# Performance work log

Measured on AMD Instinct MI355X. Metric: run time of the kernel, lower is better.

Reference implementation:

```python
import jax, jax.numpy as jnp
import numpy as np

# Model constants (from init_kwargs / _select_heads)
H = 8          # heads for dim=1024
KR = 16        # read/write top-k
CHUNK = 128    # chunk size for chunked memory update
ETA = 0.1      # update rate
FORGET = 0.01  # decay_lambda -> forget_base per chunk
LWIN = 512     # local_window = K (use_bypass=True)


def _l2norm(t, eps=1e-6):
    return t / (jnp.linalg.norm(t, axis=-1, keepdims=True) + eps)


def setup_inputs() -> dict:
    key = jax.random.key(0)
    ks = jax.random.split(key, 5)
    B, T, D, K = 2, 2048, 1024, 512
    x = jax.random.normal(ks[0], (B, T, D), dtype=jnp.float32)
    W_qkv = jax.random.normal(ks[1], (3 * D, D), dtype=jnp.float32) / np.sqrt(D)
    b_qkv = jnp.zeros((3 * D,), dtype=jnp.float32)
    W_o = jax.random.normal(ks[2], (D, D), dtype=jnp.float32) / np.sqrt(D)
    b_o = jnp.zeros((D,), dtype=jnp.float32)
    S_init = jax.random.normal(ks[3], (K, D), dtype=jnp.float32) / np.sqrt(D)
    read_temperature = jnp.ones((1,), dtype=jnp.float32)
    return {"x": x, "W_qkv": W_qkv, "b_qkv": b_qkv, "W_o": W_o,
            "b_o": b_o, "S_init": S_init, "read_temperature": read_temperature}


def reference(x, W_qkv, b_qkv, W_o, b_o, S_init, read_temperature):
    B, T, D = x.shape
    K = S_init.shape[0]
    dh = D // H
    scale = 1.0 / np.sqrt(dh)
    temp = read_temperature[0]

    # fused qkv projection, split to heads [B,H,T,dh]
    qkv = x @ W_qkv.T + b_qkv
    q, k, v = jnp.split(qkv, 3, axis=-1)
    to_h = lambda t: t.reshape(B, T, H, dh).transpose(0, 2, 1, 3)
    qh, kh, vh = to_h(q), to_h(k), to_h(v)

    # initial slot state from S_init: [K, D] -> [H, K, dh] -> [B,H,K,dh]
    slot = S_init.reshape(K, H, dh).transpose(1, 0, 2)
    slot_k0 = jnp.broadcast_to(_l2norm(slot), (B, H, K, dh))
    slot_v0 = jnp.broadcast_to(slot, (B, H, K, dh))

    nc = T // CHUNK
    # [nc, B, H, C, dh]
    to_c = lambda t: t.reshape(B, H, nc, CHUNK, dh).transpose(2, 0, 1, 3, 4)
    qc, kc, vc = to_c(qh), to_c(kh), to_c(vh)

    bi_g = jnp.arange(B)[:, None, None, None]   # gather indices
    hi_g = jnp.arange(H)[None, :, None, None]
    bi_s = jnp.arange(B)[:, None, None]         # scatter indices
    hi_s = jnp.arange(H)[None, :, None]

    def chunk_step(carry, inp):
        slot_k, slot_v = carry
        qt, kt, vt = inp  # [B,H,C,dh]
        # ---- top-k sparse read from slot memory ----
        rscores = jnp.einsum('bhcd,bhkd->bhck', qt, slot_k) * scale / temp
        rv, ri = jax.lax.top_k(rscores, KR)
        rp = jax.nn.softmax(rv, axis=-1)                 # [B,H,C,KR]
        sel_v = slot_v[bi_g, hi_g, ri]                   # [B,H,C,KR,dh]
        read = jnp.einsum('bhck,bhckd->bhcd', rp, sel_v)
        # ---- top-k write with orthogonal update + decay ----
        k_hat = _l2norm(kt)
        wscores = jnp.einsum('bhcd,bhkd->bhck', k_hat, slot_k)
        wv, wi = jax.lax.top_k(wscores, KR)
        wp = jax.nn.softmax(wv, axis=-1)
        sel_k = slot_k[bi_g, hi_g, wi]                   # [B,H,C,KR,dh]
        proj = jnp.einsum('bhcd,bhckd->bhck', vt, sel_k)
        v_orth = vt[:, :, :, None, :] - proj[..., None] * sel_k
        dv = ETA * wp[..., None] * v_orth                # [B,H,C,KR,dh]
        dk = ETA * wp[..., None] * (k_hat[:, :, :, None, :] - sel_k)
        idx = wi.reshape(B, H, CHUNK * KR)
        slot_v = (1.0 - FORGET) * slot_v
        slot_v = slot_v.at[bi_s, hi_s, idx].add(dv.reshape(B, H, CHUNK * KR, dh))
        slot_k = _l2norm(slot_k.at[bi_s, hi_s, idx].add(dk.reshape(B, H, CHUNK * KR, dh)))
        return (slot_k, slot_v), read

    _, reads = jax.lax.scan(chunk_step, (slot_k0, slot_v0), (qc, kc, vc))
    reads = reads.transpose(1, 2, 0, 3, 4).reshape(B, H, T, dh)

    # ---- local bypass: block-causal sliding-window attention (window=LWIN) ----
    nb = T // LWIN
    qb = qh.reshape(B, H, nb, LWIN, dh)
    kb = kh.reshape(B, H, nb, LWIN, dh)
    vb = vh.reshape(B, H, nb, LWIN, dh)
    zpad = jnp.zeros_like(kb[:, :, :1])
    kcat = jnp.concatenate([jnp.concatenate([zpad, kb[:, :, :-1]], axis=2), kb], axis=3)
    vcat = jnp.concatenate([jnp.concatenate([zpad, vb[:, :, :-1]], axis=2), vb], axis=3)
    s = jnp.einsum('bhnqd,bhnkd->bhnqk', qb, kcat) * scale  # [B,H,nb,LWIN,2*LWIN]
    i = jnp.arange(LWIN)[:, None]
    j = jnp.arange(2 * LWIN)[None, :]
    base = (j <= LWIN + i) & (j > i)                        # causal + window
    blk = (jnp.arange(nb) > 0)[:, None, None] | (j >= LWIN)[None]
    mask = base[None] & blk                                 # [nb,LWIN,2*LWIN]
    s = jnp.where(mask[None, None], s, -1e30)
    a = jax.nn.softmax(s, axis=-1)
    local = jnp.einsum('bhnqk,bhnkd->bhnqd', a, vcat).reshape(B, H, T, dh)

    y = (reads + local).transpose(0, 2, 1, 3).reshape(B, T, D)
    return y @ W_o.T + b_o
```

## Files before the change

kernel.cpp:

```cpp
#include <hip/hip_runtime.h>

typedef unsigned short u16;
typedef unsigned int u32;
typedef unsigned long long u64;
typedef __attribute__((ext_vector_type(8))) short bf16x8;
typedef __attribute__((ext_vector_type(4))) float f32x4;

#define B2 2
#define T2 2048
#define D2 1024
#define H2 8
#define DH 128
#define KSL 512
#define CH 128
#define NCH 16
#define NBH 16
#define MAGIC 0x13579BDFu

__device__ __forceinline__ float bf2f(u32 h) { union { u32 u; float f; } x; x.u = h << 16; return x.f; }
__device__ __forceinline__ u16 f2bf(float f) {
  union { float f; u32 u; } x; x.f = f;
  return (u16)((x.u + 0x7FFFu + ((x.u >> 16) & 1u)) >> 16);
}
__device__ __forceinline__ u32 pack2(float a, float b) { return (u32)f2bf(a) | ((u32)f2bf(b) << 16); }

__device__ __forceinline__ u32 cload32(const void* p) {
  return __hip_atomic_load((u32*)p, __ATOMIC_RELAXED, __HIP_MEMORY_SCOPE_AGENT);
}
__device__ __forceinline__ void cstore32(void* p, u32 v) {
  __hip_atomic_store((u32*)p, v, __ATOMIC_RELAXED, __HIP_MEMORY_SCOPE_AGENT);
}
__device__ __forceinline__ u64 cload64(const void* p) {
  return __hip_atomic_load((u64*)p, __ATOMIC_RELAXED, __HIP_MEMORY_SCOPE_AGENT);
}
__device__ __forceinline__ void cstore64(void* p, u64 v) {
  __hip_atomic_store((u64*)p, v, __ATOMIC_RELAXED, __HIP_MEMORY_SCOPE_AGENT);
}
__device__ __forceinline__ float2 cloadf2(const float* p) {
  union { u64 q; float2 f; } x; x.q = cload64(p); return x.f;
}
__device__ __forceinline__ void cstoref2(float* p, float2 v) {
  union { float2 f; u64 q; } x; x.f = v; cstore64(p, x.q);
}

__global__ __launch_bounds__(256) void qkv_gemm(
    const float* __restrict__ x, const float* __restrict__ w,
    const float* __restrict__ bias, u16* __restrict__ qhb,
    u16* __restrict__ khb, u16* __restrict__ vhb) {
  __shared__ u16 As[128 * 72];
  __shared__ u16 Bs[128 * 72];
  const int tid = threadIdx.x;
  const int lane = tid & 63, wv = tid >> 6;
  const int quad = lane >> 4, l15 = lane & 15;
  const int m0 = blockIdx.y * 128, n0 = blockIdx.x * 128;
  const int wr = wv >> 1, wc = wv & 1;
  f32x4 acc[4][4];
#pragma unroll
  for (int i = 0; i < 4; ++i)
#pragma unroll
    for (int j = 0; j < 4; ++j) acc[i][j] = f32x4{0.f, 0.f, 0.f, 0.f};
  const int f4c = tid & 15, r0 = tid >> 4;
  for (int kt = 0; kt < 16; ++kt) {
#pragma unroll
    for (int i = 0; i < 8; ++i) {
      int row = r0 + i * 16;
      float4 a = *(const float4*)(x + (size_t)(m0 + row) * 1024 + kt * 64 + f4c * 4);
      float4 b = *(const float4*)(w + (size_t)(n0 + row) * 1024 + kt * 64 + f4c * 4);
      *(uint2*)(&As[row * 72 + f4c * 4]) = make_uint2(pack2(a.x, a.y), pack2(a.z, a.w));
      *(uint2*)(&Bs[row * 72 + f4c * 4]) = make_uint2(pack2(b.x, b.y), pack2(b.z, b.w));
    }
    __syncthreads();
#pragma unroll
    for (int ks = 0; ks < 2; ++ks) {
      bf16x8 af[4], bff[4];
#pragma unroll
      for (int rt = 0; rt < 4; ++rt)
        af[rt] = *(const bf16x8*)(&As[(wr * 64 + rt * 16 + l15) * 72 + ks * 32 + quad * 8]);
#pragma unroll
      for (int ct = 0; ct < 4; ++ct)
        bff[ct] = *(const bf16x8*)(&Bs[(wc * 64 + ct * 16 + l15) * 72 + ks * 32 + quad * 8]);
#pragma unroll
      for (int rt = 0; rt < 4; ++rt)
#pragma unroll
        for (int ct = 0; ct < 4; ++ct)
          acc[rt][ct] = __builtin_amdgcn_mfma_f32_16x16x32_bf16(af[rt], bff[ct], acc[rt][ct], 0, 0, 0);
    }
    __syncthreads();
  }
#pragma unroll
  for (int ct = 0; ct < 4; ++ct) {
    int n = n0 + wc * 64 + ct * 16 + l15;
    float bv = bias[n];
    int sec = n >> 10, rr2 = n & 1023, hh = rr2 >> 7, dd = rr2 & 127;
    u16* dst = (sec == 0) ? qhb : (sec == 1) ? khb : vhb;
#pragma unroll
    for (int rt = 0; rt < 4; ++rt)
#pragma unroll
      for (int rg = 0; rg < 4; ++rg) {
        int m = m0 + wr * 64 + rt * 16 + quad * 4 + rg;
        int bb = m >> 11, tt = m & 2047;
        dst[((size_t)(bb * 8 + hh) * T2 + tt) * DH + dd] = f2bf(acc[rt][ct][rg] + bv);
      }
  }
}

__global__ __launch_bounds__(256) void attn_kernel(
    const u16* __restrict__ qhb, const u16* __restrict__ khb,
    const u16* __restrict__ vhb, float* __restrict__ yin) {
  __shared__ u16 Pls[128 * 72];
  __shared__ u16 VT[128 * 72];
  const int tid = threadIdx.x;
  const int lane = tid & 63, wv = tid >> 6;
  const int quad = lane >> 4, l15 = lane & 15;
  const int bh = blockIdx.y, qt = blockIdx.x;
  const int t0 = qt * 128;
  const int b = bh >> 3, h = bh & 7;
  f32x4 Oa[2][8];
  float mrow[2][4], lrow[2][4];
#pragma unroll
  for (int rt = 0; rt < 2; ++rt) {
#pragma unroll
    for (int dt = 0; dt < 8; ++dt) Oa[rt][dt] = f32x4{0.f, 0.f, 0.f, 0.f};
#pragma unroll
    for (int rg = 0; rg < 4; ++rg) { mrow[rt][rg] = -1e30f; lrow[rt][rg] = 0.f; }
  }
  const u16* qbase = qhb + ((size_t)bh * T2 + t0) * DH;
  int j0 = t0 / 64 - 8; if (j0 < 0) j0 = 0;
  int j1 = t0 / 64 + 1;
  for (int jt = j0; jt <= j1; ++jt) {
    int kv0 = jt * 64;
    __syncthreads();
    {
      int r = tid & 63, dq = tid >> 6;
      const u16* vrow = vhb + ((size_t)bh * T2 + kv0 + r) * DH + dq * 32;
#pragma unroll
      for (int u = 0; u < 4; ++u) {
        uint4 pv = *(const uint4*)(vrow + u * 8);
        int d0 = dq * 32 + u * 8;
        VT[(d0 + 0) * 72 + r] = (u16)(pv.x); VT[(d0 + 1) * 72 + r] = (u16)(pv.x >> 16);
        VT[(d0 + 2) * 72 + r] = (u16)(pv.y); VT[(d0 + 3) * 72 + r] = (u16)(pv.y >> 16);
        VT[(d0 + 4) * 72 + r] = (u16)(pv.z); VT[(d0 + 5) * 72 + r] = (u16)(pv.z >> 16);
        VT[(d0 + 6) * 72 + r] = (u16)(pv.w); VT[(d0 + 7) * 72 + r] = (u16)(pv.w >> 16);
      }
    }
    f32x4 Sa[2][4];
#pragma unroll
    for (int rt = 0; rt < 2; ++rt)
#pragma unroll
      for (int ct = 0; ct < 4; ++ct) Sa[rt][ct] = f32x4{0.f, 0.f, 0.f, 0.f};
#pragma unroll
    for (int ks = 0; ks < 4; ++ks) {
      bf16x8 a0 = *(const bf16x8*)(qbase + (size_t)(wv * 32 + l15) * DH + ks * 32 + quad * 8);
      bf16x8 a1 = *(const bf16x8*)(qbase + (size_t)(wv * 32 + 16 + l15) * DH + ks * 32 + quad * 8);
#pragma unroll
      for (int ct = 0; ct < 4; ++ct) {
        bf16x8 bb = *(const bf16x8*)(khb + ((size_t)bh * T2 + kv0 + ct * 16 + l15) * DH + ks * 32 + quad * 8);
        Sa[0][ct] = __builtin_amdgcn_mfma_f32_16x16x32_bf16(a0, bb, Sa[0][ct], 0, 0, 0);
        Sa[1][ct] = __builtin_amdgcn_mfma_f32_16x16x32_bf16(a1, bb, Sa[1][ct], 0, 0, 0);
      }
    }
#pragma unroll
    for (int rt = 0; rt < 2; ++rt)
#pragma unroll
      for (int rg = 0; rg < 4; ++rg) {
        int row = wv * 32 + rt * 16 + quad * 4 + rg;
        int qp = t0 + row;
        float vals[4];
        float mx = -1e30f;
#pragma unroll
        for (int ct = 0; ct < 4; ++ct) {
          int kp = kv0 + ct * 16 + l15;
          float s = Sa[rt][ct][rg] * 0.08838834764831845f;
          bool ok = (kp <= qp) && (kp + 512 > qp);
          s = ok ? s : -1e30f;
          vals[ct] = s;
          mx = fmaxf(mx, s);
        }
#pragma unroll
        for (int sh = 1; sh < 16; sh <<= 1) mx = fmaxf(mx, __shfl_xor(mx, sh));
        float mold = mrow[rt][rg];
        float mnew = fmaxf(mold, mx);
        float alpha = __expf(mold - mnew);
        float rsum = 0.f;
        float pv_[4];
#pragma unroll
        for (int ct = 0; ct < 4; ++ct) {
          float p = (vals[ct] < -1e29f) ? 0.f : __expf(vals[ct] - mnew);
          pv_[ct] = p; rsum += p;
        }
#pragma unroll
        for (int sh = 1; sh < 16; sh <<= 1) rsum += __shfl_xor(rsum, sh);
        lrow[rt][rg] = lrow[rt][rg] * alpha + rsum;
        mrow[rt][rg] = mnew;
#pragma unroll
        for (int dt = 0; dt < 8; ++dt) Oa[rt][dt][rg] *= alpha;
#pragma unroll
        for (int ct = 0; ct < 4; ++ct) Pls[row * 72 + ct * 16 + l15] = f2bf(pv_[ct]);
      }
    __syncthreads();
#pragma unroll
    for (int ks = 0; ks < 2; ++ks) {
      bf16x8 a0 = *(const bf16x8*)(&Pls[(wv * 32 + l15) * 72 + ks * 32 + quad * 8]);
      bf16x8 a1 = *(const bf16x8*)(&Pls[(wv * 32 + 16 + l15) * 72 + ks * 32 + quad * 8]);
#pragma unroll
      for (int dt = 0; dt < 8; ++dt) {
        bf16x8 bb = *(const bf16x8*)(&VT[(dt * 16 + l15) * 72 + ks * 32 + quad * 8]);
        Oa[0][dt] = __builtin_amdgcn_mfma_f32_16x16x32_bf16(a0, bb, Oa[0][dt], 0, 0, 0);
        Oa[1][dt] = __builtin_amdgcn_mfma_f32_16x16x32_bf16(a1, bb, Oa[1][dt], 0, 0, 0);
      }
    }
  }
#pragma unroll
  for (int rt = 0; rt < 2; ++rt)
#pragma unroll
    for (int rg = 0; rg < 4; ++rg) {
      int row = wv * 32 + rt * 16 + quad * 4 + rg;
      float invl = 1.0f / lrow[rt][rg];
#pragma unroll
      for (int dt = 0; dt < 8; ++dt)
        yin[((size_t)b * T2 + t0 + row) * D2 + h * DH + dt * 16 + l15] = Oa[rt][dt][rg] * invl;
    }
}

struct ScanArgs {
  const u16* qhb; const u16* khb; const u16* vhb;
  float* yin; float* sk; float* sv; u16* skb; u16* khatb;
  u32* cnt; uint4* entries;
  u32* barcnt; u32* bargen; u32* ready;
  const float* sinit; const float* temp;
};

__device__ __forceinline__ void bh_barrier(u32* cnt, u32* gen, bool do_inv) {
  asm volatile("" ::: "memory");
  __syncthreads();
  if (threadIdx.x == 0) {
    u32 g = cload32(gen);
    u32 a = __hip_atomic_fetch_add(cnt, 1u, __ATOMIC_RELAXED, __HIP_MEMORY_SCOPE_AGENT);
    if ((a & 15u) == 15u) {
      cstore32(gen, g + 1u);
    } else {
      while (cload32(gen) == g) __builtin_amdgcn_s_sleep(2);
    }
    if (do_inv)
      __builtin_amdgcn_fence(__ATOMIC_ACQUIRE, "agent");
  }
  __syncthreads();
  asm volatile("" ::: "memory");
}

__device__ __forceinline__ void topk16(const float* rowp, int lane, volatile u64* candw,
                                       float& p_out, u32& idx_out) {
  u32 mono[8];
#pragma unroll
  for (int j = 0; j < 8; ++j) {
    float f = rowp[j * 64 + lane];
    u32 u = __float_as_uint(f);
    mono[j] = ((int)u < 0) ? ~u : (u | 0x80000000u);
  }
  u32 mx = mono[0];
#pragma unroll
  for (int j = 1; j < 8; ++j) mx = max(mx, mono[j]);
  u32 s = mx;
#pragma unroll
  for (int k = 2; k <= 64; k <<= 1) {
#pragma unroll
    for (int j = k >> 1; j > 0; j >>= 1) {
      u32 o = (u32)__shfl_xor((int)s, j);
      bool keep_min = (((lane & k) == 0) == ((lane & j) == 0));
      u32 mn = min(s, o), mxx = max(s, o);
      s = keep_min ? mn : mxx;
    }
  }
  u32 thr = (u32)__shfl((int)s, 48);
  u32 base = 0;
#pragma unroll
  for (int j = 0; j < 8; ++j) {
    bool pred = (mono[j] >= thr);
    u64 mask = __ballot(pred);
    u32 pos = base + (u32)__popcll(mask & ((1ull << lane) - 1ull));
    if (pred && pos < 64u)
      candw[pos] = (((u64)mono[j]) << 32) | (u64)(0xFFFFFFFFu - (u32)(j * 64 + lane));
    base += (u32)__popcll(mask);
  }
  __threadfence_block();
  u32 cntc = base < 64u ? base : 64u;
  u64 key = ((u32)lane < cntc) ? candw[lane] : 0ull;
#pragma unroll
  for (int k = 2; k <= 64; k <<= 1) {
#pragma unroll
    for (int j = k >> 1; j > 0; j >>= 1) {
      u64 o = __shfl_xor(key, j);
      bool keep_min = (((lane & k) == 0) == ((lane & j) == 0));
      u64 mn = key < o ? key : o;
      u64 mxx = key < o ? o : key;
      key = keep_min ? mn : mxx;
    }
  }
  u32 um = (u32)(key >> 32);
  float val = __uint_as_float((um & 0x80000000u) ? (um & 0x7FFFFFFFu) : ~um);
  idx_out = 0xFFFFFFFFu - (u32)(key & 0xFFFFFFFFull);
  float mtop = __shfl(val, 63);
  float e = __expf(val - mtop);
  float ssum = e;
#pragma unroll
  for (int sh = 1; sh < 16; sh <<= 1) ssum += __shfl_xor(ssum, sh);
  p_out = e / ssum;
}

__global__ __launch_bounds__(512, 2) void scan_kernel(ScanArgs A) {
  const int tid = threadIdx.x;
  const int lane = tid & 63, wv = tid >> 6;
  const int quad = lane >> 4, l15 = lane & 15;
  const int xcd = blockIdx.x & 7;
  const int wi = blockIdx.x >> 3;
  const int bh = xcd * 2 + (wi >> 4);
  const int blk = wi & 15;
  const int b = bh >> 3, h = bh & 7;
  __shared__ float scores_r[8 * 520];
  __shared__ float scores_w[8 * 520];
  __shared__ u64 cand[8][64];

  const float invtemp = 1.0f / A.temp[0];
  const float sc_r = 0.08838834764831845f * invtemp;

#pragma unroll 1
  for (int i = 0; i < 4; ++i) {
    int s = blk * 32 + wv * 4 + i;
    float2 v2 = *(const float2*)(A.sinit + (size_t)s * 1024 + h * 128 + lane * 2);
    float ssq = v2.x * v2.x + v2.y * v2.y;
#pragma unroll
    for (int sh = 1; sh < 64; sh <<= 1) ssq += __shfl_xor(ssq, sh);
    float inv = 1.0f / (sqrtf(ssq) + 1e-6f);
    size_t off = ((size_t)bh * KSL + s) * DH + lane * 2;
    cstoref2(A.sk + off, make_float2(v2.x * inv, v2.y * inv));
    cstoref2(A.sv + off, v2);
    cstore32(A.skb + off, pack2(v2.x * inv, v2.y * inv));
    if (lane == 0) cstore32(&A.cnt[bh * KSL + s], 0u);
  }
#pragma unroll 1
  for (int ci = 0; ci < NCH; ++ci) {
    int trow = ci * CH + blk * 8 + wv;
    u32 kraw = *(const u32*)(A.khb + ((size_t)bh * T2 + trow) * DH + lane * 2);
    float k0 = bf2f(kraw & 0xFFFFu), k1 = bf2f(kraw >> 16);
    float ssq = k0 * k0 + k1 * k1;
#pragma unroll
    for (int sh = 1; sh < 64; sh <<= 1) ssq += __shfl_xor(ssq, sh);
    float inv = 1.0f / (sqrtf(ssq) + 1e-6f);
    cstore32(A.khatb + ((size_t)bh * T2 + trow) * DH + lane * 2, pack2(k0 * inv, k1 * inv));
  }
  if (blk == 0 && tid == 0) { cstore32(A.barcnt + bh, 0u); cstore32(A.bargen + bh, 0u); }
  __syncthreads();
  if (tid == 0) {
    cstore32(&A.ready[bh * 16 + blk], MAGIC);
    for (int i = 0; i < 16; ++i)
      while (cload32(&A.ready[bh * 16 + i]) != MAGIC) __builtin_amdgcn_s_sleep(2);
    __builtin_amdgcn_fence(__ATOMIC_ACQUIRE, "agent");
  }
  __syncthreads();

  u32* bcnt = A.barcnt + bh;
  u32* bgen = A.bargen + bh;

#pragma unroll 1
  for (int ci = 0; ci < NCH; ++ci) {
    const int t0base = ci * CH;
    const int c = blk * 8 + wv;
    const int trow = t0base + c;
    {
      const u16* qbase = A.qhb + ((size_t)bh * T2 + t0base + blk * 8) * DH;
      const u16* hbase = A.khatb + ((size_t)bh * T2 + t0base + blk * 8) * DH;
      const u16* sbase = A.skb + (size_t)bh * KSL * DH;
      f32x4 acc[4];
#pragma unroll
      for (int ct = 0; ct < 4; ++ct) acc[ct] = f32x4{0.f, 0.f, 0.f, 0.f};
#pragma unroll
      for (int ks = 0; ks < 4; ++ks) {
        bf16x8 a;
        if (l15 < 8)
          a = *(const bf16x8*)(qbase + (size_t)l15 * DH + ks * 32 + quad * 8);
        else
          a = *(const bf16x8*)(hbase + (size_t)(l15 - 8) * DH + ks * 32 + quad * 8);
#pragma unroll
        for (int ct = 0; ct < 4; ++ct) {
          bf16x8 bb = *(const bf16x8*)(sbase + (size_t)(wv * 64 + ct * 16 + l15) * DH + ks * 32 + quad * 8);
          acc[ct] = __builtin_amdgcn_mfma_f32_16x16x32_bf16(a, bb, acc[ct], 0, 0, 0);
        }
      }
#pragma unroll
      for (int ct = 0; ct < 4; ++ct)
#pragma unroll
        for (int rg = 0; rg < 4; ++rg) {
          int m = quad * 4 + rg;
          int col = wv * 64 + ct * 16 + l15;
          if (m < 8) scores_r[m * 520 + col] = acc[ct][rg] * sc_r;
          else       scores_w[(m - 8) * 520 + col] = acc[ct][rg];
        }
    }
    __syncthreads();
    {
      float p; u32 sidx;
      topk16(&scores_r[wv * 520], lane, cand[wv], p, sidx);
      float acc0 = 0.f, acc1 = 0.f;
      const float* svb = A.sv + (size_t)bh * KSL * DH;
#pragma unroll
      for (int r = 0; r < 16; ++r) {
        float pr = __shfl(p, 63 - r);
        u32 ir = (u32)__shfl((int)sidx, 63 - r);
        float2 vv = *(const float2*)(svb + (size_t)ir * DH + lane * 2);
        acc0 += pr * vv.x; acc1 += pr * vv.y;
      }
      {
        float* yp = A.yin + ((size_t)b * T2 + trow) * D2 + h * DH + lane * 2;
        float2 y0 = cloadf2(yp);
        cstoref2(yp, make_float2(y0.x + acc0, y0.y + acc1));
      }

      float wp; u32 widx;
      topk16(&scores_w[wv * 520], lane, cand[wv], wp, widx);
      const int r = lane >> 2, g = lane & 3;
      float wr = __shfl(wp, 63 - r);
      u32 ir = (u32)__shfl((int)widx, 63 - r);
      const float* kb = A.sk + ((size_t)bh * KSL + ir) * DH + g * 32;
      const u16* vb = A.vhb + ((size_t)bh * T2 + trow) * DH + g * 32;
      float part = 0.f;
#pragma unroll
      for (int u2 = 0; u2 < 4; ++u2) {
        uint4 vvp = *(const uint4*)(vb + u2 * 8);
        float4 k0 = *(const float4*)(kb + u2 * 8);
        float4 k1 = *(const float4*)(kb + u2 * 8 + 4);
        part += bf2f(vvp.x & 0xFFFFu) * k0.x + bf2f(vvp.x >> 16) * k0.y
              + bf2f(vvp.y & 0xFFFFu) * k0.z + bf2f(vvp.y >> 16) * k0.w
              + bf2f(vvp.z & 0xFFFFu) * k1.x + bf2f(vvp.z >> 16) * k1.y
              + bf2f(vvp.w & 0xFFFFu) * k1.z + bf2f(vvp.w >> 16) * k1.w;
      }
      part += __shfl_xor(part, 1);
      part += __shfl_xor(part, 2);
      if (g == 0) {
        u32 pos = __hip_atomic_fetch_add(&A.cnt[bh * KSL + ir], 1u,
                                         __ATOMIC_RELAXED, __HIP_MEMORY_SCOPE_AGENT);
        if (pos < 128u) {
          u32* e = (u32*)(A.entries + ((size_t)bh * KSL + ir) * 128 + pos);
          cstore64(e, (u64)(u32)c | ((u64)__float_as_uint(wr) << 32));
          cstore32(e + 2, __float_as_uint(part));
        }
      }
    }
    bh_barrier(bcnt, bgen, false);
    {
      u32 n4[4]; size_t soff4[4];
      uint4 eL0[4], eL1[4];
#pragma unroll
      for (int i = 0; i < 4; ++i) {
        soff4[i] = (size_t)bh * KSL + blk * 32 + wv * 4 + i;
        n4[i] = cload32(&A.cnt[soff4[i]]);
        const uint4* eb = A.entries + soff4[i] * 128;
        eL0[i] = eb[lane];
        eL1[i] = eb[64 + lane];
      }
#pragma unroll
      for (int i = 0; i < 4; ++i) {
        size_t roff = soff4[i] * DH + lane * 2;
        float2 V = *(const float2*)(A.sv + roff);
        float2 Kr = *(const float2*)(A.sk + roff);
        u32 nd = n4[i] < 128u ? n4[i] : 128u;
        float dv0 = 0, dv1 = 0, dk0 = 0, dk1 = 0;
#pragma unroll 1
        for (u32 b2 = 0; b2 < nd; b2 += 16) {
          u32 m = nd - b2; if (m > 16u) m = 16u;
          u32 sx = (b2 < 64u) ? eL0[i].x : eL1[i].x;
          u32 sy = (b2 < 64u) ? eL0[i].y : eL1[i].y;
          u32 sz = (b2 < 64u) ? eL0[i].z : eL1[i].z;
          u32 vr[16], hr[16];
#pragma unroll
          for (int j = 0; j < 16; ++j) if (j < (int)m) {
            u32 src = (b2 + (u32)j) & 63u;
            u32 c2 = (u32)__shfl((int)sx, (int)src);
            vr[j] = *(const u32*)(A.vhb + ((size_t)bh * T2 + t0base + c2) * DH + lane * 2);
            hr[j] = *(const u32*)(A.khatb + ((size_t)bh * T2 + t0base + c2) * DH + lane * 2);
          }
#pragma unroll
          for (int j = 0; j < 16; ++j) if (j < (int)m) {
            u32 src = (b2 + (u32)j) & 63u;
            float wpe = __uint_as_float((u32)__shfl((int)sy, (int)src));
            float pj = __uint_as_float((u32)__shfl((int)sz, (int)src));
            dv0 += wpe * (bf2f(vr[j] & 0xFFFFu) - pj * Kr.x);
            dv1 += wpe * (bf2f(vr[j] >> 16) - pj * Kr.y);
            dk0 += wpe * (bf2f(hr[j] & 0xFFFFu) - Kr.x);
            dk1 += wpe * (bf2f(hr[j] >> 16) - Kr.y);
          }
        }
        cstoref2(A.sv + roff, make_float2(0.99f * V.x + 0.1f * dv0, 0.99f * V.y + 0.1f * dv1));
        if (n4[i] > 0u) {
          float u0 = Kr.x + 0.1f * dk0, u1 = Kr.y + 0.1f * dk1;
          float ssq = u0 * u0 + u1 * u1;
#pragma unroll
          for (int sh = 1; sh < 64; sh <<= 1) ssq += __shfl_xor(ssq, sh);
          float inv = 1.0f / (sqrtf(ssq) + 1e-6f);
          u0 *= inv; u1 *= inv;
          cstoref2(A.sk + roff, make_float2(u0, u1));
          cstore32(A.skb + roff, pack2(u0, u1));
        }
        if (lane == 0) cstore32(&A.cnt[soff4[i]], 0u);
      }
    }
    bh_barrier(bcnt, bgen, true);
  }
}

__global__ __launch_bounds__(256) void out_gemm(
    const float* __restrict__ yin, const float* __restrict__ w,
    const float* __restrict__ bias, float* __restrict__ out) {
  __shared__ u16 As[128 * 72];
  __shared__ u16 Bs[128 * 72];
  const int tid = threadIdx.x;
  const int lane = tid & 63, wv = tid >> 6;
  const int quad = lane >> 4, l15 = lane & 15;
  const int m0 = blockIdx.y * 128, n0 = blockIdx.x * 128;
  const int wr = wv >> 1, wc = wv & 1;
  f32x4 acc[4][4];
#pragma unroll
  for (int i = 0; i < 4; ++i)
#pragma unroll
    for (int j = 0; j < 4; ++j) acc[i][j] = f32x4{0.f, 0.f, 0.f, 0.f};
  const int f4c = tid & 15, r0 = tid >> 4;
  for (int kt = 0; kt < 16; ++kt) {
#pragma unroll
    for (int i = 0; i < 8; ++i) {
      int row = r0 + i * 16;
      float4 a = *(const float4*)(yin + (size_t)(m0 + row) * 1024 + kt * 64 + f4c * 4);
      float4 b = *(const float4*)(w + (size_t)(n0 + row) * 1024 + kt * 64 + f4c * 4);
      *(uint2*)(&As[row * 72 + f4c * 4]) = make_uint2(pack2(a.x, a.y), pack2(a.z, a.w));
      *(uint2*)(&Bs[row * 72 + f4c * 4]) = make_uint2(pack2(b.x, b.y), pack2(b.z, b.w));
    }
    __syncthreads();
#pragma unroll
    for (int ks = 0; ks < 2; ++ks) {
      bf16x8 af[4], bff[4];
#pragma unroll
      for (int rt = 0; rt < 4; ++rt)
        af[rt] = *(const bf16x8*)(&As[(wr * 64 + rt * 16 + l15) * 72 + ks * 32 + quad * 8]);
#pragma unroll
      for (int ct = 0; ct < 4; ++ct)
        bff[ct] = *(const bf16x8*)(&Bs[(wc * 64 + ct * 16 + l15) * 72 + ks * 32 + quad * 8]);
#pragma unroll
      for (int rt = 0; rt < 4; ++rt)
#pragma unroll
        for (int ct = 0; ct < 4; ++ct)
          acc[rt][ct] = __builtin_amdgcn_mfma_f32_16x16x32_bf16(af[rt], bff[ct], acc[rt][ct], 0, 0, 0);
    }
    __syncthreads();
  }
#pragma unroll
  for (int ct = 0; ct < 4; ++ct) {
    int n = n0 + wc * 64 + ct * 16 + l15;
    float bv = bias[n];
#pragma unroll
    for (int rt = 0; rt < 4; ++rt)
#pragma unroll
      for (int rg = 0; rg < 4; ++rg) {
        int m = m0 + wr * 64 + rt * 16 + quad * 4 + rg;
        out[(size_t)m * 1024 + n] = acc[rt][ct][rg] + bv;
      }
  }
}

extern "C" void kernel_launch(void* const* d_in, const int* in_sizes, int n_in,
                              void* d_out, int out_size, void* d_ws, size_t ws_size,
                              hipStream_t stream) {
  const float* x = (const float*)d_in[0];
  const float* Wqkv = (const float*)d_in[1];
  const float* bqkv = (const float*)d_in[2];
  const float* Wo = (const float*)d_in[3];
  const float* bo = (const float*)d_in[4];
  const float* Sinit = (const float*)d_in[5];
  const float* temp = (const float*)d_in[6];
  float* out = (float*)d_out;

  char* p = (char*)d_ws;
  auto take = [&](size_t bytes) { char* r = p; p += (bytes + 255) & ~(size_t)255; return r; };
  u16* qhb = (u16*)take((size_t)NBH * T2 * DH * 2);
  u16* khb = (u16*)take((size_t)NBH * T2 * DH * 2);
  u16* vhb = (u16*)take((size_t)NBH * T2 * DH * 2);
  float* yin = (float*)take((size_t)B2 * T2 * D2 * 4);
  float* sk = (float*)take((size_t)NBH * KSL * DH * 4);
  float* sv = (float*)take((size_t)NBH * KSL * DH * 4);
  u16* skb = (u16*)take((size_t)NBH * KSL * DH * 2);
  u16* khatb = (u16*)take((size_t)NBH * T2 * DH * 2);
  u32* cnt = (u32*)take((size_t)NBH * KSL * 4);
  uint4* entries = (uint4*)take((size_t)NBH * KSL * 128 * 16);
  u32* barcnt = (u32*)take(64 * 4);
  u32* bargen = (u32*)take(64 * 4);
  u32* ready = (u32*)take(NBH * 16 * 4);

  hipLaunchKernelGGL(qkv_gemm, dim3(24, 32), dim3(256), 0, stream, x, Wqkv, bqkv, qhb, khb, vhb);
  hipLaunchKernelGGL(attn_kernel, dim3(16, 16), dim3(256), 0, stream, qhb, khb, vhb, yin);
  ScanArgs sa{qhb, khb, vhb, yin, sk, sv, skb, khatb, cnt, entries, barcnt, bargen, ready, Sinit, temp};
  hipLaunchKernelGGL(scan_kernel, dim3(256), dim3(512), 0, stream, sa);
  hipLaunchKernelGGL(out_gemm, dim3(8, 32), dim3(256), 0, stream, yin, Wo, bo, out);
}
```

Baseline: 678.7 us.

## Fuse local attention and memory scan into one launch running concurrently

The sliding-window attention kernel and the chunked memory scan kernel are merged into a single 512-block launch. The first 256 blocks run local attention and the rest run the scan, so the latency-bound scan overlaps with the attention work. The scan now writes its reads to a separate buffer instead of read-modify-writing the attention output, which removes the ordering dependency between the two. The output GEMM sums both buffers on load. The cost is an extra activation buffer, an extra read in the output GEMM, and attention blocks that keep half their 512 threads idle.

Result: slower. 693.6 us (+2.2%).

```diff
diff --git a/kernel.cpp b/kernel.cpp
--- a/kernel.cpp
+++ b/kernel.cpp
@@ -104,127 +104,9 @@
   }
 }
 
-__global__ __launch_bounds__(256) void attn_kernel(
-    const u16* __restrict__ qhb, const u16* __restrict__ khb,
-    const u16* __restrict__ vhb, float* __restrict__ yin) {
-  __shared__ u16 Pls[128 * 72];
-  __shared__ u16 VT[128 * 72];
-  const int tid = threadIdx.x;
-  const int lane = tid & 63, wv = tid >> 6;
-  const int quad = lane >> 4, l15 = lane & 15;
-  const int bh = blockIdx.y, qt = blockIdx.x;
-  const int t0 = qt * 128;
-  const int b = bh >> 3, h = bh & 7;
-  f32x4 Oa[2][8];
-  float mrow[2][4], lrow[2][4];
-#pragma unroll
-  for (int rt = 0; rt < 2; ++rt) {
-#pragma unroll
-    for (int dt = 0; dt < 8; ++dt) Oa[rt][dt] = f32x4{0.f, 0.f, 0.f, 0.f};
-#pragma unroll
-    for (int rg = 0; rg < 4; ++rg) { mrow[rt][rg] = -1e30f; lrow[rt][rg] = 0.f; }
-  }
-  const u16* qbase = qhb + ((size_t)bh * T2 + t0) * DH;
-  int j0 = t0 / 64 - 8; if (j0 < 0) j0 = 0;
-  int j1 = t0 / 64 + 1;
-  for (int jt = j0; jt <= j1; ++jt) {
-    int kv0 = jt * 64;
-    __syncthreads();
-    {
-      int r = tid & 63, dq = tid >> 6;
-      const u16* vrow = vhb + ((size_t)bh * T2 + kv0 + r) * DH + dq * 32;
-#pragma unroll
-      for (int u = 0; u < 4; ++u) {
-        uint4 pv = *(const uint4*)(vrow + u * 8);
-        int d0 = dq * 32 + u * 8;
-        VT[(d0 + 0) * 72 + r] = (u16)(pv.x); VT[(d0 + 1) * 72 + r] = (u16)(pv.x >> 16);
-        VT[(d0 + 2) * 72 + r] = (u16)(pv.y); VT[(d0 + 3) * 72 + r] = (u16)(pv.y >> 16);
-        VT[(d0 + 4) * 72 + r] = (u16)(pv.z); VT[(d0 + 5) * 72 + r] = (u16)(pv.z >> 16);
-        VT[(d0 + 6) * 72 + r] = (u16)(pv.w); VT[(d0 + 7) * 72 + r] = (u16)(pv.w >> 16);
-      }
-    }
-    f32x4 Sa[2][4];
-#pragma unroll
-    for (int rt = 0; rt < 2; ++rt)
-#pragma unroll
-      for (int ct = 0; ct < 4; ++ct) Sa[rt][ct] = f32x4{0.f, 0.f, 0.f, 0.f};
-#pragma unroll
-    for (int ks = 0; ks < 4; ++ks) {
-      bf16x8 a0 = *(const bf16x8*)(qbase + (size_t)(wv * 32 + l15) * DH + ks * 32 + quad * 8);
-      bf16x8 a1 = *(const bf16x8*)(qbase + (size_t)(wv * 32 + 16 + l15) * DH + ks * 32 + quad * 8);
-#pragma unroll
-      for (int ct = 0; ct < 4; ++ct) {
-        bf16x8 bb = *(const bf16x8*)(khb + ((size_t)bh * T2 + kv0 + ct * 16 + l15) * DH + ks * 32 + quad * 8);
-        Sa[0][ct] = __builtin_amdgcn_mfma_f32_16x16x32_bf16(a0, bb, Sa[0][ct], 0, 0, 0);
-        Sa[1][ct] = __builtin_amdgcn_mfma_f32_16x16x32_bf16(a1, bb, Sa[1][ct], 0, 0, 0);
-      }
-    }
-#pragma unroll
-    for (int rt = 0; rt < 2; ++rt)
-#pragma unroll
-      for (int rg = 0; rg < 4; ++rg) {
-        int row = wv * 32 + rt * 16 + quad * 4 + rg;
-        int qp = t0 + row;
-        float vals[4];
-        float mx = -1e30f;
-#pragma unroll
-        for (int ct = 0; ct < 4; ++ct) {
-          int kp = kv0 + ct * 16 + l15;
-          float s = Sa[rt][ct][rg] * 0.08838834764831845f;
-          bool ok = (kp <= qp) && (kp + 512 > qp);
-          s = ok ? s : -1e30f;
-          vals[ct] = s;
-          mx = fmaxf(mx, s);
-        }
-#pragma unroll
-        for (int sh = 1; sh < 16; sh <<= 1) mx = fmaxf(mx, __shfl_xor(mx, sh));
-        float mold = mrow[rt][rg];
-        float mnew = fmaxf(mold, mx);
-        float alpha = __expf(mold - mnew);
-        float rsum = 0.f;
-        float pv_[4];
-#pragma unroll
-        for (int ct = 0; ct < 4; ++ct) {
-          float p = (vals[ct] < -1e29f) ? 0.f : __expf(vals[ct] - mnew);
-          pv_[ct] = p; rsum += p;
-        }
-#pragma unroll
-        for (int sh = 1; sh < 16; sh <<= 1) rsum += __shfl_xor(rsum, sh);
-        lrow[rt][rg] = lrow[rt][rg] * alpha + rsum;
-        mrow[rt][rg] = mnew;
-#pragma unroll
-        for (int dt = 0; dt < 8; ++dt) Oa[rt][dt][rg] *= alpha;
-#pragma unroll
-        for (int ct = 0; ct < 4; ++ct) Pls[row * 72 + ct * 16 + l15] = f2bf(pv_[ct]);
-      }
-    __syncthreads();
-#pragma unroll
-    for (int ks = 0; ks < 2; ++ks) {
-      bf16x8 a0 = *(const bf16x8*)(&Pls[(wv * 32 + l15) * 72 + ks * 32 + quad * 8]);
-      bf16x8 a1 = *(const bf16x8*)(&Pls[(wv * 32 + 16 + l15) * 72 + ks * 32 + quad * 8]);
-#pragma unroll
-      for (int dt = 0; dt < 8; ++dt) {
-        bf16x8 bb = *(const bf16x8*)(&VT[(dt * 16 + l15) * 72 + ks * 32 + quad * 8]);
-        Oa[0][dt] = __builtin_amdgcn_mfma_f32_16x16x32_bf16(a0, bb, Oa[0][dt], 0, 0, 0);
-        Oa[1][dt] = __builtin_amdgcn_mfma_f32_16x16x32_bf16(a1, bb, Oa[1][dt], 0, 0, 0);
-      }
-    }
-  }
-#pragma unroll
-  for (int rt = 0; rt < 2; ++rt)
-#pragma unroll
-    for (int rg = 0; rg < 4; ++rg) {
-      int row = wv * 32 + rt * 16 + quad * 4 + rg;
-      float invl = 1.0f / lrow[rt][rg];
-#pragma unroll
-      for (int dt = 0; dt < 8; ++dt)
-        yin[((size_t)b * T2 + t0 + row) * D2 + h * DH + dt * 16 + l15] = Oa[rt][dt][rg] * invl;
-    }
-}
-
 struct ScanArgs {
   const u16* qhb; const u16* khb; const u16* vhb;
-  float* yin; float* sk; float* sv; u16* skb; u16* khatb;
+  float* yin; float* ys; float* sk; float* sv; u16* skb; u16* khatb;
   u32* cnt; uint4* entries;
   u32* barcnt; u32* bargen; u32* ready;
   const float* sinit; const float* temp;
@@ -307,18 +189,141 @@
   p_out = e / ssum;
 }
 
-__global__ __launch_bounds__(512, 2) void scan_kernel(ScanArgs A) {
+__global__ __launch_bounds__(512, 2) void attn_scan(ScanArgs A) {
+  __shared__ u64 smem_u64[4672];
+  char* smem = (char*)smem_u64;
   const int tid = threadIdx.x;
   const int lane = tid & 63, wv = tid >> 6;
   const int quad = lane >> 4, l15 = lane & 15;
-  const int xcd = blockIdx.x & 7;
-  const int wi = blockIdx.x >> 3;
+
+  if (blockIdx.x < 256) {
+    const int abid = blockIdx.x;
+    const int qt = abid & 15, bh = abid >> 4;
+    const int t0 = qt * 128;
+    const int b = bh >> 3, h = bh & 7;
+    int j0 = t0 / 64 - 8; if (j0 < 0) j0 = 0;
+    int j1 = t0 / 64 + 1;
+    if (tid >= 256) {
+      for (int jt = j0; jt <= j1; ++jt) { __syncthreads(); __syncthreads(); }
+      return;
+    }
+    u16* Pls = (u16*)smem;
+    u16* VT  = (u16*)(smem + 18432);
+    f32x4 Oa[2][8];
+    float mrow[2][4], lrow[2][4];
+#pragma unroll
+    for (int rt = 0; rt < 2; ++rt) {
+#pragma unroll
+      for (int dt = 0; dt < 8; ++dt) Oa[rt][dt] = f32x4{0.f, 0.f, 0.f, 0.f};
+#pragma unroll
+      for (int rg = 0; rg < 4; ++rg) { mrow[rt][rg] = -1e30f; lrow[rt][rg] = 0.f; }
+    }
+    const u16* qbase = A.qhb + ((size_t)bh * T2 + t0) * DH;
+    for (int jt = j0; jt <= j1; ++jt) {
+      int kv0 = jt * 64;
+      __syncthreads();
+      {
+        int r = tid & 63, dq = tid >> 6;
+        const u16* vrow = A.vhb + ((size_t)bh * T2 + kv0 + r) * DH + dq * 32;
+#pragma unroll
+        for (int u = 0; u < 4; ++u) {
+          uint4 pv = *(const uint4*)(vrow + u * 8);
+          int d0 = dq * 32 + u * 8;
+          VT[(d0 + 0) * 72 + r] = (u16)(pv.x); VT[(d0 + 1) * 72 + r] = (u16)(pv.x >> 16);
+          VT[(d0 + 2) * 72 + r] = (u16)(pv.y); VT[(d0 + 3) * 72 + r] = (u16)(pv.y >> 16);
+          VT[(d0 + 4) * 72 + r] = (u16)(pv.z); VT[(d0 + 5) * 72 + r] = (u16)(pv.z >> 16);
+          VT[(d0 + 6) * 72 + r] = (u16)(pv.w); VT[(d0 + 7) * 72 + r] = (u16)(pv.w >> 16);
+        }
+      }
+      f32x4 Sa[2][4];
+#pragma unroll
+      for (int rt = 0; rt < 2; ++rt)
+#pragma unroll
+        for (int ct = 0; ct < 4; ++ct) Sa[rt][ct] = f32x4{0.f, 0.f, 0.f, 0.f};
+#pragma unroll
+      for (int ks = 0; ks < 4; ++ks) {
+        bf16x8 a0 = *(const bf16x8*)(qbase + (size_t)(wv * 32 + l15) * DH + ks * 32 + quad * 8);
+        bf16x8 a1 = *(const bf16x8*)(qbase + (size_t)(wv * 32 + 16 + l15) * DH + ks * 32 + quad * 8);
+#pragma unroll
+        for (int ct = 0; ct < 4; ++ct) {
+          bf16x8 bb = *(const bf16x8*)(A.khb + ((size_t)bh * T2 + kv0 + ct * 16 + l15) * DH + ks * 32 + quad * 8);
+          Sa[0][ct] = __builtin_amdgcn_mfma_f32_16x16x32_bf16(a0, bb, Sa[0][ct], 0, 0, 0);
+          Sa[1][ct] = __builtin_amdgcn_mfma_f32_16x16x32_bf16(a1, bb, Sa[1][ct], 0, 0, 0);
+        }
+      }
+#pragma unroll
+      for (int rt = 0; rt < 2; ++rt)
+#pragma unroll
+        for (int rg = 0; rg < 4; ++rg) {
+          int row = wv * 32 + rt * 16 + quad * 4 + rg;
+          int qp = t0 + row;
+          float vals[4];
+          float mx = -1e30f;
+#pragma unroll
+          for (int ct = 0; ct < 4; ++ct) {
+            int kp = kv0 + ct * 16 + l15;
+            float s = Sa[rt][ct][rg] * 0.08838834764831845f;
+            bool ok = (kp <= qp) && (kp + 512 > qp);
+            s = ok ? s : -1e30f;
+            vals[ct] = s;
+            mx = fmaxf(mx, s);
+          }
+#pragma unroll
+          for (int sh = 1; sh < 16; sh <<= 1) mx = fmaxf(mx, __shfl_xor(mx, sh));
+          float mold = mrow[rt][rg];
+          float mnew = fmaxf(mold, mx);
+          float alpha = __expf(mold - mnew);
+          float rsum = 0.f;
+          float pv_[4];
+#pragma unroll
+          for (int ct = 0; ct < 4; ++ct) {
+            float p = (vals[ct] < -1e29f) ? 0.f : __expf(vals[ct] - mnew);
+            pv_[ct] = p; rsum += p;
+          }
+#pragma unroll
+          for (int sh = 1; sh < 16; sh <<= 1) rsum += __shfl_xor(rsum, sh);
+          lrow[rt][rg] = lrow[rt][rg] * alpha + rsum;
+          mrow[rt][rg] = mnew;
+#pragma unroll
+          for (int dt = 0; dt < 8; ++dt) Oa[rt][dt][rg] *= alpha;
+#pragma unroll
+          for (int ct = 0; ct < 4; ++ct) Pls[row * 72 + ct * 16 + l15] = f2bf(pv_[ct]);
+        }
+      __syncthreads();
+#pragma unroll
+      for (int ks = 0; ks < 2; ++ks) {
+        bf16x8 a0 = *(const bf16x8*)(&Pls[(wv * 32 + l15) * 72 + ks * 32 + quad * 8]);
+        bf16x8 a1 = *(const bf16x8*)(&Pls[(wv * 32 + 16 + l15) * 72 + ks * 32 + quad * 8]);
+#pragma unroll
+        for (int dt = 0; dt < 8; ++dt) {
+          bf16x8 bb = *(const bf16x8*)(&VT[(dt * 16 + l15) * 72 + ks * 32 + quad * 8]);
+          Oa[0][dt] = __builtin_amdgcn_mfma_f32_16x16x32_bf16(a0, bb, Oa[0][dt], 0, 0, 0);
+          Oa[1][dt] = __builtin_amdgcn_mfma_f32_16x16x32_bf16(a1, bb, Oa[1][dt], 0, 0, 0);
+        }
+      }
+    }
+#pragma unroll
+    for (int rt = 0; rt < 2; ++rt)
+#pragma unroll
+      for (int rg = 0; rg < 4; ++rg) {
+        int row = wv * 32 + rt * 16 + quad * 4 + rg;
+        float invl = 1.0f / lrow[rt][rg];
+#pragma unroll
+        for (int dt = 0; dt < 8; ++dt)
+          A.yin[((size_t)b * T2 + t0 + row) * D2 + h * DH + dt * 16 + l15] = Oa[rt][dt][rg] * invl;
+      }
+    return;
+  }
+
+  const int sb = blockIdx.x - 256;
+  const int xcd = sb & 7;
+  const int wi = sb >> 3;
   const int bh = xcd * 2 + (wi >> 4);
   const int blk = wi & 15;
   const int b = bh >> 3, h = bh & 7;
-  __shared__ float scores_r[8 * 520];
-  __shared__ float scores_w[8 * 520];
-  __shared__ u64 cand[8][64];
+  float* scores_r = (float*)smem;
+  float* scores_w = (float*)(smem + 16640);
+  u64* cand = (u64*)(smem + 33280);
 
   const float invtemp = 1.0f / A.temp[0];
   const float sc_r = 0.08838834764831845f * invtemp;
@@ -399,7 +404,7 @@
     __syncthreads();
     {
       float p; u32 sidx;
-      topk16(&scores_r[wv * 520], lane, cand[wv], p, sidx);
+      topk16(&scores_r[wv * 520], lane, cand + wv * 64, p, sidx);
       float acc0 = 0.f, acc1 = 0.f;
       const float* svb = A.sv + (size_t)bh * KSL * DH;
 #pragma unroll
@@ -409,14 +414,11 @@
         float2 vv = *(const float2*)(svb + (size_t)ir * DH + lane * 2);
         acc0 += pr * vv.x; acc1 += pr * vv.y;
       }
-      {
-        float* yp = A.yin + ((size_t)b * T2 + trow) * D2 + h * DH + lane * 2;
-        float2 y0 = cloadf2(yp);
-        cstoref2(yp, make_float2(y0.x + acc0, y0.y + acc1));
-      }
+      cstoref2(A.ys + ((size_t)b * T2 + trow) * D2 + h * DH + lane * 2,
+               make_float2(acc0, acc1));
 
       float wp; u32 widx;
-      topk16(&scores_w[wv * 520], lane, cand[wv], wp, widx);
+      topk16(&scores_w[wv * 520], lane, cand + wv * 64, wp, widx);
       const int r = lane >> 2, g = lane & 3;
       float wr = __shfl(wp, 63 - r);
       u32 ir = (u32)__shfl((int)widx, 63 - r);
@@ -508,7 +510,8 @@
 }
 
 __global__ __launch_bounds__(256) void out_gemm(
-    const float* __restrict__ yin, const float* __restrict__ w,
+    const float* __restrict__ yin, const float* __restrict__ ys,
+    const float* __restrict__ w,
     const float* __restrict__ bias, float* __restrict__ out) {
   __shared__ u16 As[128 * 72];
   __shared__ u16 Bs[128 * 72];
@@ -527,7 +530,10 @@
 #pragma unroll
     for (int i = 0; i < 8; ++i) {
       int row = r0 + i * 16;
-      float4 a = *(const float4*)(yin + (size_t)(m0 + row) * 1024 + kt * 64 + f4c * 4);
+      size_t aidx = (size_t)(m0 + row) * 1024 + kt * 64 + f4c * 4;
+      float4 a = *(const float4*)(yin + aidx);
+      float4 a2 = *(const float4*)(ys + aidx);
+      a.x += a2.x; a.y += a2.y; a.z += a2.z; a.w += a2.w;
       float4 b = *(const float4*)(w + (size_t)(n0 + row) * 1024 + kt * 64 + f4c * 4);
       *(uint2*)(&As[row * 72 + f4c * 4]) = make_uint2(pack2(a.x, a.y), pack2(a.z, a.w));
       *(uint2*)(&Bs[row * 72 + f4c * 4]) = make_uint2(pack2(b.x, b.y), pack2(b.z, b.w));
@@ -582,6 +588,7 @@
   u16* khb = (u16*)take((size_t)NBH * T2 * DH * 2);
   u16* vhb = (u16*)take((size_t)NBH * T2 * DH * 2);
   float* yin = (float*)take((size_t)B2 * T2 * D2 * 4);
+  float* ys = (float*)take((size_t)B2 * T2 * D2 * 4);
   float* sk = (float*)take((size_t)NBH * KSL * DH * 4);
   float* sv = (float*)take((size_t)NBH * KSL * DH * 4);
   u16* skb = (u16*)take((size_t)NBH * KSL * DH * 2);
@@ -593,8 +600,7 @@
   u32* ready = (u32*)take(NBH * 16 * 4);
 
   hipLaunchKernelGGL(qkv_gemm, dim3(24, 32), dim3(256), 0, stream, x, Wqkv, bqkv, qhb, khb, vhb);
-  hipLaunchKernelGGL(attn_kernel, dim3(16, 16), dim3(256), 0, stream, qhb, khb, vhb, yin);
-  ScanArgs sa{qhb, khb, vhb, yin, sk, sv, skb, khatb, cnt, entries, barcnt, bargen, ready, Sinit, temp};
-  hipLaunchKernelGGL(scan_kernel, dim3(256), dim3(512), 0, stream, sa);
-  hipLaunchKernelGGL(out_gemm, dim3(8, 32), dim3(256), 0, stream, yin, Wo, bo, out);
-}
+  ScanArgs sa{qhb, khb, vhb, yin, ys, sk, sv, skb, khatb, cnt, entries, barcnt, bargen, ready, Sinit, temp};
+  hipLaunchKernelGGL(attn_scan, dim3(512), dim3(512), 0, stream, sa);
+  hipLaunchKernelGGL(out_gemm, dim3(8, 32), dim3(256), 0, stream, yin, ys, Wo, bo, out);
+}
```
